# Kernel optimization log

Hardware: AMD Instinct MI355X
Metric: run time of the kernel (lower is better)

## Reference

```python
import jax, jax.numpy as jnp
import numpy as np
import math

N_HEADS = 16
D_HEAD = 64
DEPTH = 12
LAMBDA_INIT = 0.8 - 0.6 * math.exp(-0.3 * DEPTH)
SCALING = 1.0 / math.sqrt(D_HEAD)
RMS_EPS = 1e-6
B, T = 4, 1024


def setup_inputs() -> dict:
    key = jax.random.key(0)
    ks = jax.random.split(key, 8)
    q = jax.random.normal(ks[0], (B, 2 * N_HEADS, T, D_HEAD), dtype=jnp.float32)
    k = jax.random.normal(ks[1], (B, 2 * N_HEADS, T, D_HEAD), dtype=jnp.float32)
    v = jax.random.normal(ks[2], (B, N_HEADS, T, 2 * D_HEAD), dtype=jnp.float32)
    # causal mask, broadcast over batch/heads; masked_fill where mask == 0
    mask = jnp.tril(jnp.ones((1, 1, T, T), dtype=jnp.int32))
    lambda_q1 = 0.1 * jax.random.normal(ks[3], (N_HEADS, D_HEAD), dtype=jnp.float32)
    lambda_k1 = 0.1 * jax.random.normal(ks[4], (N_HEADS, D_HEAD), dtype=jnp.float32)
    lambda_q2 = 0.1 * jax.random.normal(ks[5], (N_HEADS, D_HEAD), dtype=jnp.float32)
    lambda_k2 = 0.1 * jax.random.normal(ks[6], (N_HEADS, D_HEAD), dtype=jnp.float32)
    rms_weight = jnp.ones((2 * D_HEAD,), dtype=jnp.float32)
    return {"q": q, "k": k, "v": v, "mask": mask,
            "lambda_q1": lambda_q1, "lambda_k1": lambda_k1,
            "lambda_q2": lambda_q2, "lambda_k2": lambda_k2,
            "rms_weight": rms_weight, "flash_attn": 0}


def _rms_norm(x, weight):
    var = jnp.mean(jnp.square(x), axis=-1, keepdims=True)
    return x * jax.lax.rsqrt(var + RMS_EPS) * weight


def reference(q, k, v, mask, lambda_q1, lambda_k1, lambda_q2, lambda_k2, rms_weight, flash_attn):
    # lambda reparameterization: scalar per head
    lambda_1 = jnp.exp(jnp.sum(lambda_q1 * lambda_k1, axis=-1))  # [H]
    lambda_2 = jnp.exp(jnp.sum(lambda_q2 * lambda_k2, axis=-1))  # [H]
    lambda_final = lambda_1 - lambda_2 + LAMBDA_INIT             # [H]

    Bq, H2, Tq, Dh = q.shape
    # dual attention scores over 2*n_heads heads: [B, 2H, T, T]
    attn = jnp.einsum('bhtd,bhsd->bhts', q, k) * SCALING
    attn = jnp.where(mask == 0, -jnp.inf, attn)
    attn = jax.nn.softmax(attn.astype(jnp.float32), axis=-1).astype(q.dtype)
    # consecutive head pairs -> (attn1, attn2)
    attn = attn.reshape(Bq, H2 // 2, 2, Tq, Tq)
    attn = attn[:, :, 0] - lambda_final[None, :, None, None] * attn[:, :, 1]
    # dropout is identity in eval mode
    y = jnp.einsum('bhts,bhsd->bhtd', attn, v)  # [B, H, T, 2*d_head]
    y = _rms_norm(y, rms_weight)
    y = y * (1.0 - LAMBDA_INIT)
    return y
```

## Files before the change

### kernel.cpp

```cpp
#include <hip/hip_runtime.h>


typedef _Float16 f16x4 __attribute__((ext_vector_type(4)));
typedef _Float16 f16x8 __attribute__((ext_vector_type(8)));
typedef float    f32x4 __attribute__((ext_vector_type(4)));

constexpr int   TSEQ        = 1024;
constexpr int   DQK         = 64;
constexpr int   DVDIM       = 128;
constexpr float SCALING     = 0.125f;
constexpr float LAMBDA_INIT = 0.7836057665316245f;
constexpr float ONE_MINUS_LI= 1.0f - LAMBDA_INIT;
constexpr float RMS_EPS     = 1e-6f;
constexpr float LOG2E       = 1.4426950408889634f;

__global__ __launch_bounds__(256, 2)
void diff_attn_kernel(const float* __restrict__ qg, const float* __restrict__ kg,
                      const float* __restrict__ vg,
                      const float* __restrict__ lq1, const float* __restrict__ lk1,
                      const float* __restrict__ lq2, const float* __restrict__ lk2,
                      const float* __restrict__ rmsw, float* __restrict__ out)
{
    __shared__ _Float16 Klds[2][2][64][72];
    __shared__ _Float16 Vt[2][128][68];

    const int hp   = blockIdx.x;
    const int a    = blockIdx.y;
    const int b    = blockIdx.z;
    const int t    = threadIdx.x;
    const int w    = t >> 6;
    const int lane = t & 63;
    const int n    = lane & 15;
    const int quad = lane >> 4;

    float a1 = lq1[hp*64 + lane] * lk1[hp*64 + lane];
    float a2 = lq2[hp*64 + lane] * lk2[hp*64 + lane];
    #pragma unroll
    for (int d = 1; d < 64; d <<= 1) { a1 += __shfl_xor(a1, d); a2 += __shfl_xor(a2, d); }
    const float lambda = __expf(a1) - __expf(a2) + LAMBDA_INIT;

    const float* kb = kg + ((size_t)(b*32 + hp*2)) * TSEQ * DQK;
    const float* vb = vg + ((size_t)(b*16 + hp))   * TSEQ * DVDIM;

    const int jj   = t & 15;
    const int sg   = t >> 4;
    const int dvb  = jj * 8;
    const int s0   = sg * 4;
    const int rotw = (jj & 7) * 8;
    const int d8   = t & 7;

    float4 kr[4][2], vr[8];

    auto load_tile = [&](int sbase) {
        #pragma unroll
        for (int i = 0; i < 4; ++i) {
            const int row = (i*256 + t) >> 3;
            const int h = row >> 6, sr = row & 63;
            const float* p = kb + ((size_t)h*TSEQ + sbase + sr)*DQK + d8*8;
            kr[i][0] = *(const float4*)p;
            kr[i][1] = *(const float4*)(p + 4);
        }
        const float* vp = vb + (size_t)(sbase + s0)*DVDIM + dvb;
        #pragma unroll
        for (int r = 0; r < 4; ++r) {
            vr[2*r]   = *(const float4*)(vp + r*DVDIM);
            vr[2*r+1] = *(const float4*)(vp + r*DVDIM + 4);
        }
    };

    auto write_tile = [&](int bi) {
        #pragma unroll
        for (int i = 0; i < 4; ++i) {
            const int row = (i*256 + t) >> 3;
            const int h = row >> 6, sr = row & 63;
            f16x8 kk;
            kk[0]=(_Float16)kr[i][0].x; kk[1]=(_Float16)kr[i][0].y;
            kk[2]=(_Float16)kr[i][0].z; kk[3]=(_Float16)kr[i][0].w;
            kk[4]=(_Float16)kr[i][1].x; kk[5]=(_Float16)kr[i][1].y;
            kk[6]=(_Float16)kr[i][1].z; kk[7]=(_Float16)kr[i][1].w;
            *(f16x8*)&Klds[bi][h][sr][d8*8] = kk;
        }
        float vrow[4][8];
        #pragma unroll
        for (int r = 0; r < 4; ++r) {
            vrow[r][0]=vr[2*r].x;   vrow[r][1]=vr[2*r].y;
            vrow[r][2]=vr[2*r].z;   vrow[r][3]=vr[2*r].w;
            vrow[r][4]=vr[2*r+1].x; vrow[r][5]=vr[2*r+1].y;
            vrow[r][6]=vr[2*r+1].z; vrow[r][7]=vr[2*r+1].w;
        }
        #pragma unroll
        for (int mI = 0; mI < 8; ++mI) {
            f16x4 pk;
            pk[0]=(_Float16)vrow[0][mI]; pk[1]=(_Float16)vrow[1][mI];
            pk[2]=(_Float16)vrow[2][mI]; pk[3]=(_Float16)vrow[3][mI];
            *(f16x4*)&Vt[bi][dvb + mI][(s0 + rotw) & 63] = pk;
        }
    };

    const float qscale = SCALING * LOG2E;

    const int A = a;
    auto seq_base = [&](int i) { return (i <= A) ? i*64 : (i - A - 1)*64; };

    load_tile(0);
    write_tile(0);
    __syncthreads();
    load_tile(seq_base(1));

    int j = 0;
    for (int part = 0; part < 2; ++part) {
        const int qt    = part ? (15 - a) : a;
        const int qbase = qt * 64;
        const int qw0   = qbase + w * 16;
        const int qrow  = qw0 + n;
        const int nT    = qt + 1;

        f16x8 Qf[2][2];
        #pragma unroll
        for (int h = 0; h < 2; ++h) {
            const float* qp = qg + (((size_t)(b*32 + hp*2 + h)) * TSEQ + qrow) * DQK + quad*8;
            #pragma unroll
            for (int ks = 0; ks < 2; ++ks) {
                float4 x = *(const float4*)(qp + ks*32);
                float4 y = *(const float4*)(qp + ks*32 + 4);
                f16x8 f;
                f[0]=(_Float16)(x.x*qscale); f[1]=(_Float16)(x.y*qscale);
                f[2]=(_Float16)(x.z*qscale); f[3]=(_Float16)(x.w*qscale);
                f[4]=(_Float16)(y.x*qscale); f[5]=(_Float16)(y.y*qscale);
                f[6]=(_Float16)(y.z*qscale); f[7]=(_Float16)(y.w*qscale);
                Qf[h][ks] = f;
            }
        }

        f32x4 O[2][8];
        #pragma unroll
        for (int h = 0; h < 2; ++h)
            #pragma unroll
            for (int d = 0; d < 8; ++d) O[h][d] = (f32x4){0.f,0.f,0.f,0.f};
        float l_[2] = { 0.f, 0.f };

        for (int tile = 0; tile < nT; ++tile, ++j) {
            const int cur   = j & 1;
            const int sbase = tile * 64;

            const bool diag = (tile == qt);
            const int  nact = diag ? (w + 1) : 4;

            f16x4 pb[2][4];
            #pragma unroll
            for (int h = 0; h < 2; ++h) {
                f32x4 St[4];
                #pragma unroll
                for (int sub = 0; sub < 4; ++sub) {
                    if (sub < nact) {
                        f16x8 k0 = *(const f16x8*)&Klds[cur][h][sub*16 + n][quad*8];
                        f16x8 k1 = *(const f16x8*)&Klds[cur][h][sub*16 + n][32 + quad*8];
                        f32x4 c = (f32x4){0.f,0.f,0.f,0.f};
                        c = __builtin_amdgcn_mfma_f32_16x16x32_f16(k0, Qf[h][0], c, 0, 0, 0);
                        c = __builtin_amdgcn_mfma_f32_16x16x32_f16(k1, Qf[h][1], c, 0, 0, 0);
                        St[sub] = c;
                    }
                }
                float rs = 0.f;
                #pragma unroll
                for (int sub = 0; sub < 4; ++sub) {
                    if (sub < nact) {
                        #pragma unroll
                        for (int r = 0; r < 4; ++r) {
                            float x = St[sub][r];
                            if (diag) {
                                const int s = sbase + sub*16 + quad*4 + r;
                                if (s > qrow) x = -__builtin_huge_valf();
                            }
                            const float p = exp2f(x);
                            rs += p;
                            pb[h][sub][r] = (_Float16)p;
                        }
                    }
                }
                l_[h] += rs;
            }

            if (j < 16) {
                write_tile(cur ^ 1);
                if (j < 15) load_tile(seq_base(j + 2));
            }

            __builtin_amdgcn_s_setprio(1);
            #pragma unroll
            for (int dd = 0; dd < 8; ++dd) {
                const int rot_r = ((2*dd + (n >> 3)) & 7) * 8;
                #pragma unroll
                for (int sub = 0; sub < 4; ++sub) {
                    if (sub < nact) {
                        f16x4 va = *(const f16x4*)&Vt[cur][dd*16 + n][(sub*16 + quad*4 + rot_r) & 63];
                        O[0][dd] = __builtin_amdgcn_mfma_f32_16x16x16f16(va, pb[0][sub], O[0][dd], 0, 0, 0);
                        O[1][dd] = __builtin_amdgcn_mfma_f32_16x16x16f16(va, pb[1][sub], O[1][dd], 0, 0, 0);
                    }
                }
            }
            __builtin_amdgcn_s_setprio(0);

            if (j < 16) __syncthreads();
        }

        float l0 = l_[0], l1 = l_[1];
        l0 += __shfl_xor(l0, 16);  l0 += __shfl_xor(l0, 32);
        l1 += __shfl_xor(l1, 16);  l1 += __shfl_xor(l1, 32);
        const float i1 = 1.0f   / l0;
        const float i2 = lambda / l1;
        float yv[8][4];
        float ss = 0.f;
        #pragma unroll
        for (int d = 0; d < 8; ++d)
            #pragma unroll
            for (int r = 0; r < 4; ++r) {
                const float y = O[0][d][r] * i1 - O[1][d][r] * i2;
                yv[d][r] = y; ss += y * y;
            }
        ss += __shfl_xor(ss, 16);
        ss += __shfl_xor(ss, 32);
        const float sc = rsqrtf(ss * (1.0f/128.0f) + RMS_EPS) * ONE_MINUS_LI;

        float* ob = out + (((size_t)(b*16 + hp)) * TSEQ + qrow) * DVDIM;
        #pragma unroll
        for (int d = 0; d < 8; ++d) {
            const int dv = d*16 + quad*4;
            float4 wv = *(const float4*)&rmsw[dv];
            float4 o;
            o.x = yv[d][0] * sc * wv.x;
            o.y = yv[d][1] * sc * wv.y;
            o.z = yv[d][2] * sc * wv.z;
            o.w = yv[d][3] * sc * wv.w;
            *(float4*)(ob + dv) = o;
        }
    }
}

extern "C" void kernel_launch(void* const* d_in, const int* in_sizes, int n_in,
                              void* d_out, int out_size, void* d_ws, size_t ws_size,
                              hipStream_t stream) {
    const float* q    = (const float*)d_in[0];
    const float* k    = (const float*)d_in[1];
    const float* v    = (const float*)d_in[2];
    const float* lq1  = (const float*)d_in[4];
    const float* lk1  = (const float*)d_in[5];
    const float* lq2  = (const float*)d_in[6];
    const float* lk2  = (const float*)d_in[7];
    const float* rmsw = (const float*)d_in[8];
    float* out = (float*)d_out;

    dim3 grid(16, 8, 4);
    dim3 block(256);
    diff_attn_kernel<<<grid, block, 0, stream>>>(q, k, v, lq1, lk1, lq2, lk2, rmsw, out);
}
```

Before: 199.3 us.

## Split head pairs across separate waves with 512-thread blocks

Doubles the block to 512 threads, so each wave handles one of the two differential heads instead of both. This halves per-wave registers and MFMA work and aims for more waves in flight. The two heads are combined at the end by having the h=1 waves write their scaled output to global memory, then a block barrier, then the h=0 waves read it back, subtract, and apply RMS norm. The tile loader is redistributed over 512 threads and the V LDS padding changes. The trade-off is an extra global write and read round trip plus a barrier in the epilogue.

```diff
diff --git a/kernel.cpp b/kernel.cpp
--- a/kernel.cpp
+++ b/kernel.cpp
@@ -1,6 +1,7 @@
 #include <hip/hip_runtime.h>
 
 
+typedef _Float16 f16x2 __attribute__((ext_vector_type(2)));
 typedef _Float16 f16x4 __attribute__((ext_vector_type(4)));
 typedef _Float16 f16x8 __attribute__((ext_vector_type(8)));
 typedef float    f32x4 __attribute__((ext_vector_type(4)));
@@ -14,7 +15,7 @@
 constexpr float RMS_EPS     = 1e-6f;
 constexpr float LOG2E       = 1.4426950408889634f;
 
-__global__ __launch_bounds__(256, 2)
+__global__ __launch_bounds__(512, 4)
 void diff_attn_kernel(const float* __restrict__ qg, const float* __restrict__ kg,
                       const float* __restrict__ vg,
                       const float* __restrict__ lq1, const float* __restrict__ lk1,
@@ -22,13 +23,15 @@
                       const float* __restrict__ rmsw, float* __restrict__ out)
 {
     __shared__ _Float16 Klds[2][2][64][72];
-    __shared__ _Float16 Vt[2][128][68];
+    __shared__ _Float16 Vt[2][128][72];
 
     const int hp   = blockIdx.x;
     const int a    = blockIdx.y;
     const int b    = blockIdx.z;
     const int t    = threadIdx.x;
-    const int w    = t >> 6;
+    const int wid  = t >> 6;
+    const int h    = wid & 1;
+    const int qgi  = wid >> 1;
     const int lane = t & 63;
     const int n    = lane & 15;
     const int quad = lane >> 4;
@@ -42,58 +45,46 @@
     const float* kb = kg + ((size_t)(b*32 + hp*2)) * TSEQ * DQK;
     const float* vb = vg + ((size_t)(b*16 + hp))   * TSEQ * DVDIM;
 
-    const int jj   = t & 15;
-    const int sg   = t >> 4;
-    const int dvb  = jj * 8;
-    const int s0   = sg * 4;
-    const int rotw = (jj & 7) * 8;
-    const int d8   = t & 7;
-
-    float4 kr[4][2], vr[8];
+    const int d16 = t & 15;
+    const int jj  = t & 15;
+    const int sg  = t >> 4;
+    const int dvb = jj * 8;
+    const int s0  = sg * 2;
+    const int rotw= (jj & 7) * 8;
+
+    float4 kr[4], vr[4];
 
     auto load_tile = [&](int sbase) {
         #pragma unroll
         for (int i = 0; i < 4; ++i) {
-            const int row = (i*256 + t) >> 3;
-            const int h = row >> 6, sr = row & 63;
-            const float* p = kb + ((size_t)h*TSEQ + sbase + sr)*DQK + d8*8;
-            kr[i][0] = *(const float4*)p;
-            kr[i][1] = *(const float4*)(p + 4);
+            const int row = i*32 + (t >> 4);
+            const int h2 = row >> 6, sr = row & 63;
+            kr[i] = *(const float4*)(kb + ((size_t)h2*TSEQ + sbase + sr)*DQK + d16*4);
         }
         const float* vp = vb + (size_t)(sbase + s0)*DVDIM + dvb;
-        #pragma unroll
-        for (int r = 0; r < 4; ++r) {
-            vr[2*r]   = *(const float4*)(vp + r*DVDIM);
-            vr[2*r+1] = *(const float4*)(vp + r*DVDIM + 4);
-        }
+        vr[0] = *(const float4*)(vp);
+        vr[1] = *(const float4*)(vp + 4);
+        vr[2] = *(const float4*)(vp + DVDIM);
+        vr[3] = *(const float4*)(vp + DVDIM + 4);
     };
 
     auto write_tile = [&](int bi) {
         #pragma unroll
         for (int i = 0; i < 4; ++i) {
-            const int row = (i*256 + t) >> 3;
-            const int h = row >> 6, sr = row & 63;
-            f16x8 kk;
-            kk[0]=(_Float16)kr[i][0].x; kk[1]=(_Float16)kr[i][0].y;
-            kk[2]=(_Float16)kr[i][0].z; kk[3]=(_Float16)kr[i][0].w;
-            kk[4]=(_Float16)kr[i][1].x; kk[5]=(_Float16)kr[i][1].y;
-            kk[6]=(_Float16)kr[i][1].z; kk[7]=(_Float16)kr[i][1].w;
-            *(f16x8*)&Klds[bi][h][sr][d8*8] = kk;
-        }
-        float vrow[4][8];
-        #pragma unroll
-        for (int r = 0; r < 4; ++r) {
-            vrow[r][0]=vr[2*r].x;   vrow[r][1]=vr[2*r].y;
-            vrow[r][2]=vr[2*r].z;   vrow[r][3]=vr[2*r].w;
-            vrow[r][4]=vr[2*r+1].x; vrow[r][5]=vr[2*r+1].y;
-            vrow[r][6]=vr[2*r+1].z; vrow[r][7]=vr[2*r+1].w;
-        }
+            const int row = i*32 + (t >> 4);
+            const int h2 = row >> 6, sr = row & 63;
+            f16x4 kk;
+            kk[0]=(_Float16)kr[i].x; kk[1]=(_Float16)kr[i].y;
+            kk[2]=(_Float16)kr[i].z; kk[3]=(_Float16)kr[i].w;
+            *(f16x4*)&Klds[bi][h2][sr][d16*4] = kk;
+        }
+        const int col = (s0 + rotw) & 63;
         #pragma unroll
         for (int mI = 0; mI < 8; ++mI) {
-            f16x4 pk;
-            pk[0]=(_Float16)vrow[0][mI]; pk[1]=(_Float16)vrow[1][mI];
-            pk[2]=(_Float16)vrow[2][mI]; pk[3]=(_Float16)vrow[3][mI];
-            *(f16x4*)&Vt[bi][dvb + mI][(s0 + rotw) & 63] = pk;
+            const float x0 = (mI < 4) ? ((const float*)&vr[0])[mI] : ((const float*)&vr[1])[mI-4];
+            const float x1 = (mI < 4) ? ((const float*)&vr[2])[mI] : ((const float*)&vr[3])[mI-4];
+            f16x2 pk; pk[0] = (_Float16)x0; pk[1] = (_Float16)x1;
+            *(f16x2*)&Vt[bi][dvb + mI][col] = pk;
         }
     };
 
@@ -109,15 +100,12 @@
 
     int j = 0;
     for (int part = 0; part < 2; ++part) {
-        const int qt    = part ? (15 - a) : a;
-        const int qbase = qt * 64;
-        const int qw0   = qbase + w * 16;
-        const int qrow  = qw0 + n;
-        const int nT    = qt + 1;
-
-        f16x8 Qf[2][2];
-        #pragma unroll
-        for (int h = 0; h < 2; ++h) {
+        const int qt   = part ? (15 - a) : a;
+        const int qrow = qt*64 + qgi*16 + n;
+        const int nT   = qt + 1;
+
+        f16x8 Qf[2];
+        {
             const float* qp = qg + (((size_t)(b*32 + hp*2 + h)) * TSEQ + qrow) * DQK + quad*8;
             #pragma unroll
             for (int ks = 0; ks < 2; ++ks) {
@@ -128,58 +116,52 @@
                 f[2]=(_Float16)(x.z*qscale); f[3]=(_Float16)(x.w*qscale);
                 f[4]=(_Float16)(y.x*qscale); f[5]=(_Float16)(y.y*qscale);
                 f[6]=(_Float16)(y.z*qscale); f[7]=(_Float16)(y.w*qscale);
-                Qf[h][ks] = f;
-            }
-        }
-
-        f32x4 O[2][8];
-        #pragma unroll
-        for (int h = 0; h < 2; ++h)
-            #pragma unroll
-            for (int d = 0; d < 8; ++d) O[h][d] = (f32x4){0.f,0.f,0.f,0.f};
-        float l_[2] = { 0.f, 0.f };
+                Qf[ks] = f;
+            }
+        }
+
+        f32x4 O[8];
+        #pragma unroll
+        for (int d = 0; d < 8; ++d) O[d] = (f32x4){0.f,0.f,0.f,0.f};
+        float l_ = 0.f;
 
         for (int tile = 0; tile < nT; ++tile, ++j) {
             const int cur   = j & 1;
             const int sbase = tile * 64;
-
             const bool diag = (tile == qt);
-            const int  nact = diag ? (w + 1) : 4;
-
-            f16x4 pb[2][4];
-            #pragma unroll
-            for (int h = 0; h < 2; ++h) {
-                f32x4 St[4];
-                #pragma unroll
-                for (int sub = 0; sub < 4; ++sub) {
-                    if (sub < nact) {
-                        f16x8 k0 = *(const f16x8*)&Klds[cur][h][sub*16 + n][quad*8];
-                        f16x8 k1 = *(const f16x8*)&Klds[cur][h][sub*16 + n][32 + quad*8];
-                        f32x4 c = (f32x4){0.f,0.f,0.f,0.f};
-                        c = __builtin_amdgcn_mfma_f32_16x16x32_f16(k0, Qf[h][0], c, 0, 0, 0);
-                        c = __builtin_amdgcn_mfma_f32_16x16x32_f16(k1, Qf[h][1], c, 0, 0, 0);
-                        St[sub] = c;
+            const int  nact = diag ? (qgi + 1) : 4;
+
+            f16x4 pb[4];
+            f32x4 St[4];
+            #pragma unroll
+            for (int sub = 0; sub < 4; ++sub) {
+                if (sub < nact) {
+                    f16x8 k0 = *(const f16x8*)&Klds[cur][h][sub*16 + n][quad*8];
+                    f16x8 k1 = *(const f16x8*)&Klds[cur][h][sub*16 + n][32 + quad*8];
+                    f32x4 c = (f32x4){0.f,0.f,0.f,0.f};
+                    c = __builtin_amdgcn_mfma_f32_16x16x32_f16(k0, Qf[0], c, 0, 0, 0);
+                    c = __builtin_amdgcn_mfma_f32_16x16x32_f16(k1, Qf[1], c, 0, 0, 0);
+                    St[sub] = c;
+                }
+            }
+            float rs = 0.f;
+            #pragma unroll
+            for (int sub = 0; sub < 4; ++sub) {
+                if (sub < nact) {
+                    #pragma unroll
+                    for (int r = 0; r < 4; ++r) {
+                        float x = St[sub][r];
+                        if (diag) {
+                            const int s = sbase + sub*16 + quad*4 + r;
+                            if (s > qrow) x = -__builtin_huge_valf();
+                        }
+                        const float p = exp2f(x);
+                        rs += p;
+                        pb[sub][r] = (_Float16)p;
                     }
                 }
-                float rs = 0.f;
-                #pragma unroll
-                for (int sub = 0; sub < 4; ++sub) {
-                    if (sub < nact) {
-                        #pragma unroll
-                        for (int r = 0; r < 4; ++r) {
-                            float x = St[sub][r];
-                            if (diag) {
-                                const int s = sbase + sub*16 + quad*4 + r;
-                                if (s > qrow) x = -__builtin_huge_valf();
-                            }
-                            const float p = exp2f(x);
-                            rs += p;
-                            pb[h][sub][r] = (_Float16)p;
-                        }
-                    }
-                }
-                l_[h] += rs;
-            }
+            }
+            l_ += rs;
 
             if (j < 16) {
                 write_tile(cur ^ 1);
@@ -194,8 +176,7 @@
                 for (int sub = 0; sub < 4; ++sub) {
                     if (sub < nact) {
                         f16x4 va = *(const f16x4*)&Vt[cur][dd*16 + n][(sub*16 + quad*4 + rot_r) & 63];
-                        O[0][dd] = __builtin_amdgcn_mfma_f32_16x16x16f16(va, pb[0][sub], O[0][dd], 0, 0, 0);
-                        O[1][dd] = __builtin_amdgcn_mfma_f32_16x16x16f16(va, pb[1][sub], O[1][dd], 0, 0, 0);
+                        O[dd] = __builtin_amdgcn_mfma_f32_16x16x16f16(va, pb[sub], O[dd], 0, 0, 0);
                     }
                 }
             }
@@ -204,35 +185,49 @@
             if (j < 16) __syncthreads();
         }
 
-        float l0 = l_[0], l1 = l_[1];
-        l0 += __shfl_xor(l0, 16);  l0 += __shfl_xor(l0, 32);
-        l1 += __shfl_xor(l1, 16);  l1 += __shfl_xor(l1, 32);
-        const float i1 = 1.0f   / l0;
-        const float i2 = lambda / l1;
-        float yv[8][4];
-        float ss = 0.f;
-        #pragma unroll
-        for (int d = 0; d < 8; ++d)
-            #pragma unroll
-            for (int r = 0; r < 4; ++r) {
-                const float y = O[0][d][r] * i1 - O[1][d][r] * i2;
-                yv[d][r] = y; ss += y * y;
-            }
-        ss += __shfl_xor(ss, 16);
-        ss += __shfl_xor(ss, 32);
-        const float sc = rsqrtf(ss * (1.0f/128.0f) + RMS_EPS) * ONE_MINUS_LI;
+        l_ += __shfl_xor(l_, 16);
+        l_ += __shfl_xor(l_, 32);
 
         float* ob = out + (((size_t)(b*16 + hp)) * TSEQ + qrow) * DVDIM;
-        #pragma unroll
-        for (int d = 0; d < 8; ++d) {
-            const int dv = d*16 + quad*4;
-            float4 wv = *(const float4*)&rmsw[dv];
-            float4 o;
-            o.x = yv[d][0] * sc * wv.x;
-            o.y = yv[d][1] * sc * wv.y;
-            o.z = yv[d][2] * sc * wv.z;
-            o.w = yv[d][3] * sc * wv.w;
-            *(float4*)(ob + dv) = o;
+        if (h == 1) {
+            const float s1 = lambda / l_;
+            #pragma unroll
+            for (int d = 0; d < 8; ++d) {
+                float4 o;
+                o.x = O[d][0]*s1; o.y = O[d][1]*s1;
+                o.z = O[d][2]*s1; o.w = O[d][3]*s1;
+                *(float4*)(ob + d*16 + quad*4) = o;
+            }
+        }
+        __syncthreads();
+        if (h == 0) {
+            const float i1 = 1.0f / l_;
+            float yv[8][4];
+            float ss = 0.f;
+            #pragma unroll
+            for (int d = 0; d < 8; ++d) {
+                const float4 y1 = *(const float4*)(ob + d*16 + quad*4);
+                yv[d][0] = O[d][0]*i1 - y1.x;
+                yv[d][1] = O[d][1]*i1 - y1.y;
+                yv[d][2] = O[d][2]*i1 - y1.z;
+                yv[d][3] = O[d][3]*i1 - y1.w;
+                ss += yv[d][0]*yv[d][0] + yv[d][1]*yv[d][1]
+                    + yv[d][2]*yv[d][2] + yv[d][3]*yv[d][3];
+            }
+            ss += __shfl_xor(ss, 16);
+            ss += __shfl_xor(ss, 32);
+            const float sc = rsqrtf(ss * (1.0f/128.0f) + RMS_EPS) * ONE_MINUS_LI;
+            #pragma unroll
+            for (int d = 0; d < 8; ++d) {
+                const int dv = d*16 + quad*4;
+                const float4 wv = *(const float4*)&rmsw[dv];
+                float4 o;
+                o.x = yv[d][0] * sc * wv.x;
+                o.y = yv[d][1] * sc * wv.y;
+                o.z = yv[d][2] * sc * wv.z;
+                o.w = yv[d][3] * sc * wv.w;
+                *(float4*)(ob + dv) = o;
+            }
         }
     }
 }
@@ -251,6 +246,6 @@
     float* out = (float*)d_out;
 
     dim3 grid(16, 8, 4);
-    dim3 block(256);
+    dim3 block(512);
     diff_attn_kernel<<<grid, block, 0, stream>>>(q, k, v, lq1, lk1, lq2, lk2, rmsw, out);
 }
```

Measured after the change: 263.7 us. 32.3% more time.

## Fuse both causal query tiles into one pass over shared K/V tiles

Applied to the files above, without the earlier changes.

Each block used to make two sequential passes over K/V, one for its low query tile and one for its high query tile. It now holds both query tiles' Q fragments and output accumulators at once and streams K/V a single time. Each loaded tile feeds both query tiles, with the low tile active only up to its diagonal, so the redundant reload of early K/V tiles and the extra barriers go away. The prefetch buffers are converted to fp16 at load time, with scheduling barriers to batch the global loads, and the tile index is remapped by batch to vary per-block work. The cost is doubled accumulator and Q register state, which raises register pressure and could cause spills or lower occupancy.

```diff
diff --git a/kernel.cpp b/kernel.cpp
--- a/kernel.cpp
+++ b/kernel.cpp
@@ -21,12 +21,15 @@
                       const float* __restrict__ lq2, const float* __restrict__ lk2,
                       const float* __restrict__ rmsw, float* __restrict__ out)
 {
-    __shared__ _Float16 Klds[2][2][64][72];
-    __shared__ _Float16 Vt[2][128][68];
+    __shared__ __align__(16) _Float16 Klds[2][2][64][72];
+    __shared__ __align__(16) _Float16 Vt[2][128][68];
 
     const int hp   = blockIdx.x;
-    const int a    = blockIdx.y;
+    const int y    = blockIdx.y;
     const int b    = blockIdx.z;
+    const int a    = (b < 2) ? y : (7 - y);
+    const int nU   = 16 - a;
+    const int qtL  = a, qtH = 15 - a;
     const int t    = threadIdx.x;
     const int w    = t >> 6;
     const int lane = t & 63;
@@ -49,162 +52,230 @@
     const int rotw = (jj & 7) * 8;
     const int d8   = t & 7;
 
-    float4 kr[4][2], vr[8];
+    f16x8 krh[4];
+    f16x4 vrh[8];
+
+    auto cvt8 = [](float4 x, float4 y2) {
+        f16x8 f;
+        f[0]=(_Float16)x.x;  f[1]=(_Float16)x.y;  f[2]=(_Float16)x.z;  f[3]=(_Float16)x.w;
+        f[4]=(_Float16)y2.x; f[5]=(_Float16)y2.y; f[6]=(_Float16)y2.z; f[7]=(_Float16)y2.w;
+        return f;
+    };
 
     auto load_tile = [&](int sbase) {
+        #pragma unroll
+        for (int i = 0; i < 4; i += 2) {
+            const int row0 = (i*256 + t) >> 3;
+            const int row1 = ((i+1)*256 + t) >> 3;
+            const float* p0 = kb + ((size_t)(row0 >> 6)*TSEQ + sbase + (row0 & 63))*DQK + d8*8;
+            const float* p1 = kb + ((size_t)(row1 >> 6)*TSEQ + sbase + (row1 & 63))*DQK + d8*8;
+            float4 x0 = *(const float4*)p0;
+            float4 x1 = *(const float4*)(p0 + 4);
+            float4 x2 = *(const float4*)p1;
+            float4 x3 = *(const float4*)(p1 + 4);
+            __builtin_amdgcn_sched_barrier(0);
+            krh[i]   = cvt8(x0, x1);
+            krh[i+1] = cvt8(x2, x3);
+        }
+        const float* vp = vb + (size_t)(sbase + s0)*DVDIM + dvb;
+        #pragma unroll
+        for (int r = 0; r < 4; r += 2) {
+            float4 x0 = *(const float4*)(vp + r*DVDIM);
+            float4 x1 = *(const float4*)(vp + r*DVDIM + 4);
+            float4 x2 = *(const float4*)(vp + (r+1)*DVDIM);
+            float4 x3 = *(const float4*)(vp + (r+1)*DVDIM + 4);
+            __builtin_amdgcn_sched_barrier(0);
+            f16x4 lo, hi;
+            lo[0]=(_Float16)x0.x; lo[1]=(_Float16)x0.y; lo[2]=(_Float16)x0.z; lo[3]=(_Float16)x0.w;
+            hi[0]=(_Float16)x1.x; hi[1]=(_Float16)x1.y; hi[2]=(_Float16)x1.z; hi[3]=(_Float16)x1.w;
+            vrh[2*r]   = lo;
+            vrh[2*r+1] = hi;
+            lo[0]=(_Float16)x2.x; lo[1]=(_Float16)x2.y; lo[2]=(_Float16)x2.z; lo[3]=(_Float16)x2.w;
+            hi[0]=(_Float16)x3.x; hi[1]=(_Float16)x3.y; hi[2]=(_Float16)x3.z; hi[3]=(_Float16)x3.w;
+            vrh[2*r+2] = lo;
+            vrh[2*r+3] = hi;
+        }
+    };
+
+    auto write_tile = [&](int bi) {
         #pragma unroll
         for (int i = 0; i < 4; ++i) {
             const int row = (i*256 + t) >> 3;
-            const int h = row >> 6, sr = row & 63;
-            const float* p = kb + ((size_t)h*TSEQ + sbase + sr)*DQK + d8*8;
-            kr[i][0] = *(const float4*)p;
-            kr[i][1] = *(const float4*)(p + 4);
-        }
-        const float* vp = vb + (size_t)(sbase + s0)*DVDIM + dvb;
-        #pragma unroll
-        for (int r = 0; r < 4; ++r) {
-            vr[2*r]   = *(const float4*)(vp + r*DVDIM);
-            vr[2*r+1] = *(const float4*)(vp + r*DVDIM + 4);
+            const int h2 = row >> 6, sr = row & 63;
+            *(f16x8*)&Klds[bi][h2][sr][d8*8] = krh[i];
+        }
+        #pragma unroll
+        for (int mI = 0; mI < 8; ++mI) {
+            const int jx = mI >> 2, e = mI & 3;
+            f16x4 pk;
+            pk[0] = vrh[0 + jx][e];
+            pk[1] = vrh[2 + jx][e];
+            pk[2] = vrh[4 + jx][e];
+            pk[3] = vrh[6 + jx][e];
+            *(f16x4*)&Vt[bi][dvb + mI][(s0 + rotw) & 63] = pk;
         }
     };
 
-    auto write_tile = [&](int bi) {
-        #pragma unroll
-        for (int i = 0; i < 4; ++i) {
-            const int row = (i*256 + t) >> 3;
-            const int h = row >> 6, sr = row & 63;
-            f16x8 kk;
-            kk[0]=(_Float16)kr[i][0].x; kk[1]=(_Float16)kr[i][0].y;
-            kk[2]=(_Float16)kr[i][0].z; kk[3]=(_Float16)kr[i][0].w;
-            kk[4]=(_Float16)kr[i][1].x; kk[5]=(_Float16)kr[i][1].y;
-            kk[6]=(_Float16)kr[i][1].z; kk[7]=(_Float16)kr[i][1].w;
-            *(f16x8*)&Klds[bi][h][sr][d8*8] = kk;
-        }
-        float vrow[4][8];
-        #pragma unroll
-        for (int r = 0; r < 4; ++r) {
-            vrow[r][0]=vr[2*r].x;   vrow[r][1]=vr[2*r].y;
-            vrow[r][2]=vr[2*r].z;   vrow[r][3]=vr[2*r].w;
-            vrow[r][4]=vr[2*r+1].x; vrow[r][5]=vr[2*r+1].y;
-            vrow[r][6]=vr[2*r+1].z; vrow[r][7]=vr[2*r+1].w;
-        }
-        #pragma unroll
-        for (int mI = 0; mI < 8; ++mI) {
-            f16x4 pk;
-            pk[0]=(_Float16)vrow[0][mI]; pk[1]=(_Float16)vrow[1][mI];
-            pk[2]=(_Float16)vrow[2][mI]; pk[3]=(_Float16)vrow[3][mI];
-            *(f16x4*)&Vt[bi][dvb + mI][(s0 + rotw) & 63] = pk;
-        }
-    };
-
     const float qscale = SCALING * LOG2E;
-
-    const int A = a;
-    auto seq_base = [&](int i) { return (i <= A) ? i*64 : (i - A - 1)*64; };
+    const int   qrowL  = qtL*64 + w*16 + n;
+    const int   qrowH  = qtH*64 + w*16 + n;
+
+    f16x8 QfL[2][2], QfH[2][2];
+    #pragma unroll
+    for (int h = 0; h < 2; ++h) {
+        const float* qpL = qg + (((size_t)(b*32 + hp*2 + h)) * TSEQ + qrowL) * DQK + quad*8;
+        const float* qpH = qg + (((size_t)(b*32 + hp*2 + h)) * TSEQ + qrowH) * DQK + quad*8;
+        #pragma unroll
+        for (int ks = 0; ks < 2; ++ks) {
+            float4 x = *(const float4*)(qpL + ks*32);
+            float4 z = *(const float4*)(qpL + ks*32 + 4);
+            f16x8 f;
+            f[0]=(_Float16)(x.x*qscale); f[1]=(_Float16)(x.y*qscale);
+            f[2]=(_Float16)(x.z*qscale); f[3]=(_Float16)(x.w*qscale);
+            f[4]=(_Float16)(z.x*qscale); f[5]=(_Float16)(z.y*qscale);
+            f[6]=(_Float16)(z.z*qscale); f[7]=(_Float16)(z.w*qscale);
+            QfL[h][ks] = f;
+            x = *(const float4*)(qpH + ks*32);
+            z = *(const float4*)(qpH + ks*32 + 4);
+            f[0]=(_Float16)(x.x*qscale); f[1]=(_Float16)(x.y*qscale);
+            f[2]=(_Float16)(x.z*qscale); f[3]=(_Float16)(x.w*qscale);
+            f[4]=(_Float16)(z.x*qscale); f[5]=(_Float16)(z.y*qscale);
+            f[6]=(_Float16)(z.z*qscale); f[7]=(_Float16)(z.w*qscale);
+            QfH[h][ks] = f;
+        }
+    }
+
+    f32x4 OL[2][8], OH[2][8];
+    #pragma unroll
+    for (int h = 0; h < 2; ++h)
+        #pragma unroll
+        for (int d = 0; d < 8; ++d) {
+            OL[h][d] = (f32x4){0.f,0.f,0.f,0.f};
+            OH[h][d] = (f32x4){0.f,0.f,0.f,0.f};
+        }
+    float lL[2] = {0.f, 0.f}, lH[2] = {0.f, 0.f};
 
     load_tile(0);
     write_tile(0);
     __syncthreads();
-    load_tile(seq_base(1));
-
-    int j = 0;
-    for (int part = 0; part < 2; ++part) {
-        const int qt    = part ? (15 - a) : a;
-        const int qbase = qt * 64;
-        const int qw0   = qbase + w * 16;
-        const int qrow  = qw0 + n;
-        const int nT    = qt + 1;
-
-        f16x8 Qf[2][2];
+    if (nU > 1) load_tile(64);
+
+    for (int j = 0; j < nU; ++j) {
+        const int  cur   = j & 1;
+        const int  sbase = j * 64;
+        const bool loAct = (j <= qtL);
+        const bool dL = (j == qtL), dH = (j == qtH);
+        const int  nactL = dL ? (w + 1) : 4;
+        const int  nactH = dH ? (w + 1) : 4;
+
+        f16x4 pbL[2][4], pbH[2][4];
+
         #pragma unroll
         for (int h = 0; h < 2; ++h) {
-            const float* qp = qg + (((size_t)(b*32 + hp*2 + h)) * TSEQ + qrow) * DQK + quad*8;
-            #pragma unroll
-            for (int ks = 0; ks < 2; ++ks) {
-                float4 x = *(const float4*)(qp + ks*32);
-                float4 y = *(const float4*)(qp + ks*32 + 4);
-                f16x8 f;
-                f[0]=(_Float16)(x.x*qscale); f[1]=(_Float16)(x.y*qscale);
-                f[2]=(_Float16)(x.z*qscale); f[3]=(_Float16)(x.w*qscale);
-                f[4]=(_Float16)(y.x*qscale); f[5]=(_Float16)(y.y*qscale);
-                f[6]=(_Float16)(y.z*qscale); f[7]=(_Float16)(y.w*qscale);
-                Qf[h][ks] = f;
-            }
-        }
-
-        f32x4 O[2][8];
-        #pragma unroll
-        for (int h = 0; h < 2; ++h)
-            #pragma unroll
-            for (int d = 0; d < 8; ++d) O[h][d] = (f32x4){0.f,0.f,0.f,0.f};
-        float l_[2] = { 0.f, 0.f };
-
-        for (int tile = 0; tile < nT; ++tile, ++j) {
-            const int cur   = j & 1;
-            const int sbase = tile * 64;
-
-            const bool diag = (tile == qt);
-            const int  nact = diag ? (w + 1) : 4;
-
-            f16x4 pb[2][4];
+            f32x4 St[4];
+            #pragma unroll
+            for (int sub = 0; sub < 4; ++sub) {
+                if (sub < nactH) {
+                    f16x8 k0 = *(const f16x8*)&Klds[cur][h][sub*16 + n][quad*8];
+                    f16x8 k1 = *(const f16x8*)&Klds[cur][h][sub*16 + n][32 + quad*8];
+                    f32x4 c = (f32x4){0.f,0.f,0.f,0.f};
+                    c = __builtin_amdgcn_mfma_f32_16x16x32_f16(k0, QfH[h][0], c, 0, 0, 0);
+                    c = __builtin_amdgcn_mfma_f32_16x16x32_f16(k1, QfH[h][1], c, 0, 0, 0);
+                    St[sub] = c;
+                }
+            }
+            float rs = 0.f;
+            #pragma unroll
+            for (int sub = 0; sub < 4; ++sub) {
+                if (sub < nactH) {
+                    #pragma unroll
+                    for (int r = 0; r < 4; ++r) {
+                        float x = St[sub][r];
+                        if (dH) {
+                            const int s = sbase + sub*16 + quad*4 + r;
+                            if (s > qrowH) x = -__builtin_huge_valf();
+                        }
+                        const float p = exp2f(x);
+                        rs += p;
+                        pbH[h][sub][r] = (_Float16)p;
+                    }
+                }
+            }
+            lH[h] += rs;
+        }
+        if (loAct) {
             #pragma unroll
             for (int h = 0; h < 2; ++h) {
                 f32x4 St[4];
                 #pragma unroll
                 for (int sub = 0; sub < 4; ++sub) {
-                    if (sub < nact) {
+                    if (sub < nactL) {
                         f16x8 k0 = *(const f16x8*)&Klds[cur][h][sub*16 + n][quad*8];
                         f16x8 k1 = *(const f16x8*)&Klds[cur][h][sub*16 + n][32 + quad*8];
                         f32x4 c = (f32x4){0.f,0.f,0.f,0.f};
-                        c = __builtin_amdgcn_mfma_f32_16x16x32_f16(k0, Qf[h][0], c, 0, 0, 0);
-                        c = __builtin_amdgcn_mfma_f32_16x16x32_f16(k1, Qf[h][1], c, 0, 0, 0);
+                        c = __builtin_amdgcn_mfma_f32_16x16x32_f16(k0, QfL[h][0], c, 0, 0, 0);
+                        c = __builtin_amdgcn_mfma_f32_16x16x32_f16(k1, QfL[h][1], c, 0, 0, 0);
                         St[sub] = c;
                     }
                 }
                 float rs = 0.f;
                 #pragma unroll
                 for (int sub = 0; sub < 4; ++sub) {
-                    if (sub < nact) {
+                    if (sub < nactL) {
                         #pragma unroll
                         for (int r = 0; r < 4; ++r) {
                             float x = St[sub][r];
-                            if (diag) {
+                            if (dL) {
                                 const int s = sbase + sub*16 + quad*4 + r;
-                                if (s > qrow) x = -__builtin_huge_valf();
+                                if (s > qrowL) x = -__builtin_huge_valf();
                             }
                             const float p = exp2f(x);
                             rs += p;
-                            pb[h][sub][r] = (_Float16)p;
+                            pbL[h][sub][r] = (_Float16)p;
                         }
                     }
                 }
-                l_[h] += rs;
-            }
-
-            if (j < 16) {
-                write_tile(cur ^ 1);
-                if (j < 15) load_tile(seq_base(j + 2));
-            }
-
-            __builtin_amdgcn_s_setprio(1);
-            #pragma unroll
-            for (int dd = 0; dd < 8; ++dd) {
-                const int rot_r = ((2*dd + (n >> 3)) & 7) * 8;
-                #pragma unroll
-                for (int sub = 0; sub < 4; ++sub) {
-                    if (sub < nact) {
-                        f16x4 va = *(const f16x4*)&Vt[cur][dd*16 + n][(sub*16 + quad*4 + rot_r) & 63];
-                        O[0][dd] = __builtin_amdgcn_mfma_f32_16x16x16f16(va, pb[0][sub], O[0][dd], 0, 0, 0);
-                        O[1][dd] = __builtin_amdgcn_mfma_f32_16x16x16f16(va, pb[1][sub], O[1][dd], 0, 0, 0);
-                    }
-                }
-            }
-            __builtin_amdgcn_s_setprio(0);
-
-            if (j < 16) __syncthreads();
-        }
-
-        float l0 = l_[0], l1 = l_[1];
+                lL[h] += rs;
+            }
+        }
+
+        if (j + 1 < nU) {
+            write_tile(cur ^ 1);
+            if (j + 2 < nU) load_tile((j + 2) * 64);
+        }
+
+        __builtin_amdgcn_s_setprio(1);
+        #pragma unroll
+        for (int dd = 0; dd < 8; ++dd) {
+            const int rot_r = ((2*dd + (n >> 3)) & 7) * 8;
+            #pragma unroll
+            for (int sub = 0; sub < 4; ++sub) {
+                const bool needH = (sub < nactH);
+                const bool needL = loAct && (sub < nactL);
+                if (needH || needL) {
+                    f16x4 va = *(const f16x4*)&Vt[cur][dd*16 + n][(sub*16 + quad*4 + rot_r) & 63];
+                    if (needH) {
+                        OH[0][dd] = __builtin_amdgcn_mfma_f32_16x16x16f16(va, pbH[0][sub], OH[0][dd], 0, 0, 0);
+                        OH[1][dd] = __builtin_amdgcn_mfma_f32_16x16x16f16(va, pbH[1][sub], OH[1][dd], 0, 0, 0);
+                    }
+                    if (needL) {
+                        OL[0][dd] = __builtin_amdgcn_mfma_f32_16x16x16f16(va, pbL[0][sub], OL[0][dd], 0, 0, 0);
+                        OL[1][dd] = __builtin_amdgcn_mfma_f32_16x16x16f16(va, pbL[1][sub], OL[1][dd], 0, 0, 0);
+                    }
+                }
+            }
+        }
+        __builtin_amdgcn_s_setprio(0);
+
+        if (j + 1 < nU) __syncthreads();
+    }
+
+    #pragma unroll
+    for (int e = 0; e < 2; ++e) {
+        f32x4 (&O)[2][8] = e ? OL : OH;
+        float l0 = e ? lL[0] : lH[0];
+        float l1 = e ? lL[1] : lH[1];
+        const int qrow = e ? qrowL : qrowH;
         l0 += __shfl_xor(l0, 16);  l0 += __shfl_xor(l0, 32);
         l1 += __shfl_xor(l1, 16);  l1 += __shfl_xor(l1, 32);
         const float i1 = 1.0f   / l0;
@@ -215,8 +286,8 @@
         for (int d = 0; d < 8; ++d)
             #pragma unroll
             for (int r = 0; r < 4; ++r) {
-                const float y = O[0][d][r] * i1 - O[1][d][r] * i2;
-                yv[d][r] = y; ss += y * y;
+                const float yy = O[0][d][r] * i1 - O[1][d][r] * i2;
+                yv[d][r] = yy; ss += yy * yy;
             }
         ss += __shfl_xor(ss, 16);
         ss += __shfl_xor(ss, 32);
@@ -226,7 +297,7 @@
         #pragma unroll
         for (int d = 0; d < 8; ++d) {
             const int dv = d*16 + quad*4;
-            float4 wv = *(const float4*)&rmsw[dv];
+            const float4 wv = *(const float4*)&rmsw[dv];
             float4 o;
             o.x = yv[d][0] * sc * wv.x;
             o.y = yv[d][1] * sc * wv.y;
```

Measured after the change: 353.6 us. 1.77x slower.
